# Performance work log

Hardware: AMD Instinct MI355X
Metric: run time of the kernel (lower is better)

## Reference

```python
import jax, jax.numpy as jnp
import numpy as np

B, C, T = 4, 512, 4096
N2 = 32          # d_state // 2 complex modes
H = 2048         # hidden_channels
EPS = 1e-5


def setup_inputs() -> dict:
    key = jax.random.key(0)
    ks = jax.random.split(key, 8)
    dt_min, dt_max = 1e-3, 1e-1
    log_dt = jax.random.uniform(ks[1], (C,)) * (np.log(dt_max) - np.log(dt_min)) + np.log(dt_min)
    return {
        "x": jax.random.normal(ks[0], (B, C, T), jnp.float32),
        # ChannelwiseLayerNorm affine params
        "gamma": jnp.ones((C,), jnp.float32),
        "beta": jnp.zeros((C,), jnp.float32),
        # S4D kernel params (standard S4D-Lin init)
        "log_dt": log_dt.astype(jnp.float32),
        "C_re": jax.random.normal(ks[2], (C, N2), jnp.float32),
        "C_im": jax.random.normal(ks[3], (C, N2), jnp.float32),
        "log_A_real": jnp.log(0.5 * jnp.ones((C, N2), jnp.float32)),
        "A_imag": jnp.tile(jnp.pi * jnp.arange(N2, dtype=jnp.float32), (C, 1)),
        "D": jax.random.normal(ks[4], (C,), jnp.float32),
        # S4D output linear (Conv1d k=1 -> 2C, then GLU over channels)
        "Wo": jax.random.normal(ks[5], (2 * C, C), jnp.float32) / np.sqrt(C),
        "bo": jnp.zeros((2 * C,), jnp.float32),
        # FC MLP: Linear(C->H), PReLU(H), Linear(H->C)
        "W1": jax.random.normal(ks[6], (H, C), jnp.float32) / np.sqrt(C),
        "b1": jnp.zeros((H,), jnp.float32),
        "prelu_a": 0.25 * jnp.ones((H,), jnp.float32),
        "W2": jax.random.normal(ks[7], (C, H), jnp.float32) / np.sqrt(H),
        "b2": jnp.zeros((C,), jnp.float32),
    }


def reference(x, gamma, beta, log_dt, C_re, C_im, log_A_real, A_imag, D,
              Wo, bo, W1, b1, prelu_a, W2, b2):
    # ---- ChannelwiseLayerNorm over the channel dim of [B, C, T] ----
    mean = jnp.mean(x, axis=1, keepdims=True)
    var = jnp.var(x, axis=1, keepdims=True)
    u = gamma[None, :, None] * (x - mean) * jax.lax.rsqrt(var + EPS) + beta[None, :, None]

    # ---- S4D: diagonal SSM kernel via Vandermonde, applied by FFT conv ----
    L = x.shape[-1]
    dt = jnp.exp(log_dt)[:, None]                       # [C, 1]
    A = -jnp.exp(log_A_real) + 1j * A_imag              # [C, N2] complex diag
    dtA = A * dt                                        # [C, N2]
    Cd = (C_re + 1j * C_im) * (jnp.exp(dtA) - 1.0) / A  # discretized C (ZOH)
    vand = jnp.exp(dtA[..., None] * jnp.arange(L, dtype=jnp.float32))  # [C, N2, L]
    K = 2.0 * jnp.einsum('hn,hnl->hl', Cd, vand).real   # [C, L]

    k_f = jnp.fft.rfft(K, n=2 * L)                      # [C, L+1]
    u_f = jnp.fft.rfft(u, n=2 * L)                      # [B, C, L+1]
    y = jnp.fft.irfft(u_f * k_f, n=2 * L)[..., :L]      # causal conv
    y = y + u * D[None, :, None]                        # skip connection
    y = jax.nn.gelu(y, approximate=False)
    # output linear (1x1 conv to 2C) + GLU over channel dim
    z = jnp.einsum('oc,bct->bot', Wo, y) + bo[None, :, None]
    y = z[:, :C] * jax.nn.sigmoid(z[:, C:])             # [B, C, T]

    # ---- FC MLP with PReLU (per hidden channel) ----
    y = y.transpose(0, 2, 1)                            # [B, T, C]
    h = y @ W1.T + b1                                   # [B, T, H]
    h = jnp.where(h >= 0, h, prelu_a * h)
    y = h @ W2.T + b2                                   # [B, T, C]

    return x + y.transpose(0, 2, 1)                     # residual, [B, C, T]
```

## Files before the change

### kernel.cpp

```cpp
#include <hip/hip_runtime.h>
#include <math.h>

#define BB 4
#define CC 512
#define TT 4096
#define NN2 32
#define HH 2048

typedef __bf16 bf8v __attribute__((ext_vector_type(8)));
typedef __bf16 bf4v __attribute__((ext_vector_type(4)));
typedef float  f4v  __attribute__((ext_vector_type(4)));
typedef unsigned short u16x8 __attribute__((ext_vector_type(8)));

__device__ __forceinline__ void gload16(const void* g, void* l){
  __builtin_amdgcn_global_load_lds(
      (const __attribute__((address_space(1))) unsigned int*)g,
      (__attribute__((address_space(3))) unsigned int*)l, 16, 0, 0);
}
__device__ __forceinline__ float fast_gelu(float v){
  float x2 = v*v;
  float x  = 0.7978845608f*v*fmaf(0.044715f, x2, 1.0f);
  float t  = __expf(2.0f*x);
  return v - v*__builtin_amdgcn_rcpf(1.0f + t);
}
__device__ __forceinline__ float fast_sigmoid(float g){
  return __builtin_amdgcn_rcpf(1.0f + __expf(-g));
}
__device__ __forceinline__ unsigned short bfbits(float v){
  __bf16 h = (__bf16)v;
  return __builtin_bit_cast(unsigned short, h);
}

__global__ __launch_bounds__(256) void ln_kernel(
    const float* __restrict__ x, const float* __restrict__ gamma,
    const float* __restrict__ beta, __bf16* __restrict__ u)
{
  int tile = blockIdx.x & 127;
  int b    = blockIdx.x >> 7;
  int tsl = threadIdx.x & 7;
  int cg  = threadIdx.x >> 3;
  const float4* xp = (const float4*)(x + (size_t)b*CC*TT + tile*32) + tsl;
  float4 cv[16];
  float4 s = {0,0,0,0}, s2 = {0,0,0,0};
  #pragma unroll
  for (int j = 0; j < 16; ++j){
    float4 v = xp[(size_t)(cg*16 + j)*(TT/4)];
    cv[j] = v;
    s.x += v.x; s.y += v.y; s.z += v.z; s.w += v.w;
    s2.x = fmaf(v.x,v.x,s2.x); s2.y = fmaf(v.y,v.y,s2.y);
    s2.z = fmaf(v.z,v.z,s2.z); s2.w = fmaf(v.w,v.w,s2.w);
  }
  __shared__ float4 ls[32][8], ls2[32][8], mean_s[8], inv_s[8];
  ls[cg][tsl] = s; ls2[cg][tsl] = s2;
  __syncthreads();
  if (threadIdx.x < 8){
    float4 ss = {0,0,0,0}, ss2 = {0,0,0,0};
    #pragma unroll
    for (int g2 = 0; g2 < 32; ++g2){
      float4 a = ls[g2][threadIdx.x], b2 = ls2[g2][threadIdx.x];
      ss.x+=a.x; ss.y+=a.y; ss.z+=a.z; ss.w+=a.w;
      ss2.x+=b2.x; ss2.y+=b2.y; ss2.z+=b2.z; ss2.w+=b2.w;
    }
    float4 mn, iv;
    mn.x = ss.x*(1.f/CC); mn.y = ss.y*(1.f/CC); mn.z = ss.z*(1.f/CC); mn.w = ss.w*(1.f/CC);
    iv.x = rsqrtf(ss2.x*(1.f/CC) - mn.x*mn.x + 1e-5f);
    iv.y = rsqrtf(ss2.y*(1.f/CC) - mn.y*mn.y + 1e-5f);
    iv.z = rsqrtf(ss2.z*(1.f/CC) - mn.z*mn.z + 1e-5f);
    iv.w = rsqrtf(ss2.w*(1.f/CC) - mn.w*mn.w + 1e-5f);
    mean_s[threadIdx.x] = mn; inv_s[threadIdx.x] = iv;
  }
  __syncthreads();
  float4 mn = mean_s[tsl], iv = inv_s[tsl];
  __bf16* up = u + (size_t)b*CC*TT + tile*32 + tsl*4;
  #pragma unroll
  for (int j = 0; j < 16; ++j){
    int c = cg*16 + j;
    float4 v = cv[j];
    float gi = gamma[c], be = beta[c];
    bf4v o;
    o[0] = (__bf16)fmaf(gi*iv.x, v.x - mn.x, be);
    o[1] = (__bf16)fmaf(gi*iv.y, v.y - mn.y, be);
    o[2] = (__bf16)fmaf(gi*iv.z, v.z - mn.z, be);
    o[3] = (__bf16)fmaf(gi*iv.w, v.w - mn.w, be);
    *(bf4v*)&up[(size_t)c*TT] = o;
  }
}

__global__ __launch_bounds__(256) void build_mats(
    const float* __restrict__ log_dt, const float* __restrict__ C_re,
    const float* __restrict__ C_im, const float* __restrict__ log_A_real,
    const float* __restrict__ A_imag, const float* __restrict__ Dp,
    __bf16* __restrict__ Tt, __bf16* __restrict__ V, __bf16* __restrict__ B2)
{
  __shared__ float cpart[4][64][33];
  __shared__ float kk[4][65];
  const int wv = threadIdx.x >> 6, lane = threadIdx.x & 63;
  const int c = blockIdx.x*4 + wv;
  const int m = lane & 31;
  float dt = expf(log_dt[c]);
  float Ar = -expf(log_A_real[c*NN2+m]);
  float Ai = A_imag[c*NN2+m];
  float er = expf(Ar*dt);
  float sw_, cw_; sincosf(Ai*dt, &sw_, &cw_);
  float wre = er*cw_, wim = er*sw_;
  float nr = wre-1.f, ni = wim;
  float inv = 1.f/(Ar*Ar + Ai*Ai);
  float qr = (nr*Ar + ni*Ai)*inv;
  float qi = (ni*Ar - nr*Ai)*inv;
  float Cr = C_re[c*NN2+m], Ci = C_im[c*NN2+m];
  float okr =  2.f*(Cr*qr - Ci*qi);
  float oki = -2.f*(Cr*qi + Ci*qr);
  __bf16* Ttc = Tt + (size_t)c*4096;
  __bf16* Vc  = V  + (size_t)c*4096;
  __bf16* B2c = B2 + (size_t)c*4096;
  if (lane < 32){
    float pre = 1.f, pim = 0.f;
    for (int l = 0; l <= 64; ++l){
      if (l <= 63){
        Vc[(2*m)*64   + (63-l)] = (__bf16)pre;
        Vc[(2*m+1)*64 + (63-l)] = (__bf16)pim;
      }
      float cR = fmaf(okr, pre,  oki*pim);
      float cQ = fmaf(oki, pre, -okr*pim);
      if (l <= 63) cpart[wv][l][m] = cR;
      if (l >= 1){
        B2c[(l-1)*64 + 2*m]   = (__bf16)cR;
        B2c[(l-1)*64 + 2*m+1] = (__bf16)cQ;
      }
      float npre = wre*pre - wim*pim;
      float npim = wre*pim + wim*pre;
      pre = npre; pim = npim;
    }
  }
  __syncthreads();
  float s = 0.f;
  #pragma unroll
  for (int mm = 0; mm < 32; ++mm) s += cpart[wv][lane][mm];
  if (lane == 0) s += Dp[c];
  kk[wv][lane] = s;
  __syncthreads();
  const int n = lane;
  #pragma unroll
  for (int kb = 0; kb < 8; ++kb){
    u16x8 v;
    #pragma unroll
    for (int e = 0; e < 8; ++e){
      int k = kb*8 + e;
      v[e] = bfbits((n >= k) ? kk[wv][n-k] : 0.f);
    }
    *(u16x8*)&Ttc[n*64 + kb*8] = v;
  }
}

__global__ __launch_bounds__(128) void s4dm_kernel(
    const __bf16* __restrict__ u, const float* __restrict__ log_dt,
    const float* __restrict__ log_A_real, const float* __restrict__ A_imag,
    const __bf16* __restrict__ Tt, const __bf16* __restrict__ V,
    const __bf16* __restrict__ B2, __bf16* __restrict__ gout)
{
  __shared__ __align__(16) float gbuf[2][64][66];
  __shared__ __align__(16) unsigned short s0buf[2][64][72];
  const int wv = threadIdx.x >> 6, l = threadIdx.x & 63;
  const int lr = l & 15, q = l >> 4;
  const int seq = blockIdx.x*2 + wv;
  const int c = seq & (CC-1);
  const __bf16* Up  = u  + (size_t)seq*TT;
  const __bf16* Ttc = Tt + (size_t)c*4096;
  const __bf16* Vc  = V  + (size_t)c*4096;
  const __bf16* B2c = B2 + (size_t)c*4096;

  f4v acc[4][4];
  #pragma unroll
  for (int a=0;a<4;++a)
    #pragma unroll
    for (int b=0;b<4;++b)
      #pragma unroll
      for (int r=0;r<4;++r) acc[a][b][r] = 0.f;

  #pragma unroll
  for (int kw = 0; kw < 2; ++kw){
    bf8v af[4], bv[4];
    #pragma unroll
    for (int mt=0;mt<4;++mt)
      af[mt] = *(const bf8v*)(Up + (mt*16+lr)*64 + kw*32 + q*8);
    #pragma unroll
    for (int nt=0;nt<4;++nt)
      bv[nt] = *(const bf8v*)(Vc + (nt*16+lr)*64 + kw*32 + q*8);
    #pragma unroll
    for (int mt=0;mt<4;++mt)
      #pragma unroll
      for (int nt=0;nt<4;++nt)
        acc[mt][nt] = __builtin_amdgcn_mfma_f32_16x16x32_bf16(af[mt], bv[nt], acc[mt][nt], 0,0,0);
  }
  #pragma unroll
  for (int mt=0;mt<4;++mt)
    #pragma unroll
    for (int nt=0;nt<4;++nt)
      #pragma unroll
      for (int r=0;r<4;++r)
        gbuf[wv][mt*16 + q*4 + r][nt*16 + lr] = acc[mt][nt][r];
  __syncthreads();

  if (l < 32){
    const int m = l;
    float dt = expf(log_dt[c]);
    float Ar = -expf(log_A_real[c*NN2+m]);
    float Ai = A_imag[c*NN2+m];
    float er = expf(Ar*dt);
    float sw_, cw_; sincosf(Ai*dt, &sw_, &cw_);
    float wr_ = er*cw_, wi_ = er*sw_;
    #pragma unroll
    for (int sq2=0;sq2<6;++sq2){
      float a=wr_, b=wi_;
      wr_ = a*a - b*b; wi_ = 2.f*a*b;
    }
    float S0r=0.f, S0i=0.f;
    for (int j=0;j<64;++j){
      float gr = gbuf[wv][j][2*m], gi = gbuf[wv][j][2*m+1];
      s0buf[wv][j][2*m]   = bfbits(S0r);
      s0buf[wv][j][2*m+1] = bfbits(S0i);
      float nRe = fmaf(wr_, S0r, fmaf(-wi_, S0i, gr));
      float nIm = fmaf(wr_, S0i, fmaf( wi_, S0r, gi));
      S0r = nRe; S0i = nIm;
    }
  }
  __syncthreads();

  #pragma unroll
  for (int a=0;a<4;++a)
    #pragma unroll
    for (int b=0;b<4;++b)
      #pragma unroll
      for (int r=0;r<4;++r) acc[a][b][r] = 0.f;
  #pragma unroll
  for (int kw = 0; kw < 2; ++kw){
    bf8v af[4], bv[4];
    #pragma unroll
    for (int mt=0;mt<4;++mt)
      af[mt] = *(const bf8v*)(Up + (mt*16+lr)*64 + kw*32 + q*8);
    #pragma unroll
    for (int nt=0;nt<4;++nt)
      bv[nt] = *(const bf8v*)(Ttc + (nt*16+lr)*64 + kw*32 + q*8);
    #pragma unroll
    for (int mt=0;mt<4;++mt)
      #pragma unroll
      for (int nt=0;nt<4;++nt)
        acc[mt][nt] = __builtin_amdgcn_mfma_f32_16x16x32_bf16(af[mt], bv[nt], acc[mt][nt], 0,0,0);
  }
  #pragma unroll
  for (int kw = 0; kw < 2; ++kw){
    bf8v af[4], bv[4];
    #pragma unroll
    for (int mt=0;mt<4;++mt)
      af[mt] = *(const bf8v*)&s0buf[wv][mt*16+lr][kw*32 + q*8];
    #pragma unroll
    for (int nt=0;nt<4;++nt)
      bv[nt] = *(const bf8v*)(B2c + (nt*16+lr)*64 + kw*32 + q*8);
    #pragma unroll
    for (int mt=0;mt<4;++mt)
      #pragma unroll
      for (int nt=0;nt<4;++nt)
        acc[mt][nt] = __builtin_amdgcn_mfma_f32_16x16x32_bf16(af[mt], bv[nt], acc[mt][nt], 0,0,0);
  }
  __syncthreads();

  unsigned short (*ybuf)[72] = (unsigned short(*)[72])&gbuf[wv][0][0];
  #pragma unroll
  for (int mt=0;mt<4;++mt)
    #pragma unroll
    for (int nt=0;nt<4;++nt)
      #pragma unroll
      for (int r=0;r<4;++r)
        ybuf[mt*16 + q*4 + r][nt*16 + lr] = bfbits(fast_gelu(acc[mt][nt][r]));
  __syncthreads();
  u16x8* dst = (u16x8*)(gout + (size_t)seq*TT);
  for (int i = l; i < 512; i += 64){
    int row = i >> 3, cq = i & 7;
    dst[i] = *(const u16x8*)&ybuf[row][cq*8];
  }
}

__global__ __launch_bounds__(256) void tr_kernel(const __bf16* __restrict__ gin,
                                                 __bf16* __restrict__ gout)
{
  __shared__ __align__(16) unsigned short ts[64][72];
  int bt = blockIdx.x;
  int bc = blockIdx.y;
  int b  = blockIdx.z;
  int tid = threadIdx.x;
  const __bf16* gp = gin + ((size_t)b*CC + bc*64)*TT + (size_t)bt*64;
  for (int i = tid; i < 512; i += 256){
    int c = i >> 3, tq = i & 7;
    u16x8 v = *(const u16x8*)(gp + (size_t)c*TT + tq*8);
    #pragma unroll
    for (int s = 0; s < 8; ++s) ts[tq*8+s][c] = v[s];
  }
  __syncthreads();
  __bf16* op = gout + ((size_t)b*TT + bt*64)*CC + bc*64;
  for (int i = tid; i < 512; i += 256){
    int t = i >> 3, cq = i & 7;
    u16x8 v = *(const u16x8*)&ts[t][cq*8];
    *(u16x8*)(op + (size_t)t*CC + cq*8) = v;
  }
}

__global__ __launch_bounds__(256) void cvt_kernel(const float4* __restrict__ in,
                                                  bf4v* __restrict__ out, int n4)
{
  int i = blockIdx.x*256 + threadIdx.x;
  if (i < n4){
    float4 v = in[i];
    bf4v o; o[0]=(__bf16)v.x; o[1]=(__bf16)v.y; o[2]=(__bf16)v.z; o[3]=(__bf16)v.w;
    out[i] = o;
  }
}

template<int MODE>
__global__ __launch_bounds__(256) void mm_kernel(
    const __bf16* __restrict__ Aw, const __bf16* __restrict__ Bt,
    const float* __restrict__ bias, const float* __restrict__ aux,
    void* __restrict__ outp)
{
  constexpr int K  = (MODE==2) ? 2048 : 512;
  constexpr int NT = K/64;
  constexpr int LOGGM = (MODE==1) ? 4 : 2;
  constexpr int GM = 1 << LOGGM;

  __shared__ __align__(16) __bf16 As[128*64];
  __shared__ __align__(16) __bf16 Bs[128*64];
  __shared__ __align__(16) __bf16 As2[(MODE==0)?128*64:8];

  const int bid = blockIdx.x;
  const int X = bid & 7, L = bid >> 3;
  const int m0 = (L & (GM-1)) * 128;
  const int n0 = (X*16 + (L >> LOGGM)) * 128;

  const int tid = threadIdx.x;
  const int l = tid & 63;
  const int lr = l & 15, kh = l >> 4;
  const int w = tid >> 6;
  const int wr = w >> 1, wc = w & 1;
  const int swk = lr & 7;

  f4v acc[4][4];
  f4v acc2[(MODE==0)?4:1][(MODE==0)?4:1];
  #pragma unroll
  for (int a=0;a<4;++a)
    #pragma unroll
    for (int b=0;b<4;++b)
      #pragma unroll
      for (int r=0;r<4;++r) acc[a][b][r] = 0.f;
  if constexpr (MODE==0){
    #pragma unroll
    for (int a=0;a<4;++a)
      #pragma unroll
      for (int b=0;b<4;++b)
        #pragma unroll
        for (int r=0;r<4;++r) acc2[a][b][r] = 0.f;
  }

  const char* pA  = (const char*)Aw;
  const char* pA2 = (const char*)(Aw + (size_t)CC*K);
  const char* pB  = (const char*)Bt;

  int offA[4], offB[4];
  #pragma unroll
  for (int i = 0; i < 4; ++i){
    int cch = i*256 + tid;
    int row = cch >> 3;
    int pos = cch & 7;
    int qq  = pos ^ (row & 7);
    offA[i] = ((m0 + row)*K + qq*8)*2;
    offB[i] = ((n0 + row)*K + qq*8)*2;
  }

  #pragma unroll 1
  for (int kt = 0; kt < NT; ++kt){
    #pragma unroll
    for (int i = 0; i < 4; ++i){
      int cch = i*256 + tid;
      gload16(pA + (size_t)offA[i] + kt*128, (char*)As + cch*16);
      gload16(pB + (size_t)offB[i] + kt*128, (char*)Bs + cch*16);
      if constexpr (MODE==0)
        gload16(pA2 + (size_t)offA[i] + kt*128, (char*)As2 + cch*16);
    }
    __syncthreads();

    #pragma unroll
    for (int kk2 = 0; kk2 < 2; ++kk2){
      const int coff = ((kk2*4 + kh) ^ swk) * 16;
      bf8v af[4], bv4[4];
      #pragma unroll
      for (int mi=0;mi<4;++mi){
        int row = wr*64 + mi*16 + lr;
        af[mi] = *(const bf8v*)((const char*)As + row*128 + coff);
      }
      #pragma unroll
      for (int ni=0;ni<4;++ni){
        int row = wc*64 + ni*16 + lr;
        bv4[ni] = *(const bf8v*)((const char*)Bs + row*128 + coff);
      }
      if constexpr (MODE==0){
        bf8v af2[4];
        #pragma unroll
        for (int mi=0;mi<4;++mi){
          int row = wr*64 + mi*16 + lr;
          af2[mi] = *(const bf8v*)((const char*)As2 + row*128 + coff);
        }
        #pragma unroll
        for (int mi=0;mi<4;++mi)
          #pragma unroll
          for (int ni=0;ni<4;++ni){
            acc [mi][ni] = __builtin_amdgcn_mfma_f32_16x16x32_bf16(af [mi], bv4[ni], acc [mi][ni], 0,0,0);
            acc2[mi][ni] = __builtin_amdgcn_mfma_f32_16x16x32_bf16(af2[mi], bv4[ni], acc2[mi][ni], 0,0,0);
          }
      } else {
        #pragma unroll
        for (int mi=0;mi<4;++mi)
          #pragma unroll
          for (int ni=0;ni<4;++ni)
            acc[mi][ni] = __builtin_amdgcn_mfma_f32_16x16x32_bf16(af[mi], bv4[ni], acc[mi][ni], 0,0,0);
      }
    }
    __syncthreads();
  }

  if constexpr (MODE==0 || MODE==1){
    const int COUT = (MODE==0) ? CC : HH;
    __bf16* O = (__bf16*)outp;
    #pragma unroll
    for (int mi=0;mi<4;++mi){
      int m = m0 + wr*64 + mi*16 + kh*4;
      float4 bi = *(const float4*)&bias[m];
      float bia[4] = {bi.x, bi.y, bi.z, bi.w};
      float gta[4], paa[4];
      if constexpr (MODE==0){
        float4 bg = *(const float4*)&bias[CC + m];
        gta[0]=bg.x; gta[1]=bg.y; gta[2]=bg.z; gta[3]=bg.w;
      } else {
        float4 pa = *(const float4*)&aux[m];
        paa[0]=pa.x; paa[1]=pa.y; paa[2]=pa.z; paa[3]=pa.w;
      }
      #pragma unroll
      for (int ni=0;ni<4;++ni){
        int tok = n0 + wc*64 + ni*16 + lr;
        bf4v o;
        #pragma unroll
        for (int r=0;r<4;++r){
          float v = acc[mi][ni][r] + bia[r];
          if constexpr (MODE==0){
            float gate = acc2[mi][ni][r] + gta[r];
            v = v * fast_sigmoid(gate);
          } else {
            v = (v >= 0.f) ? v : paa[r]*v;
          }
          o[r] = (__bf16)v;
        }
        *(bf4v*)&O[(size_t)tok*COUT + m] = o;
      }
    }
  } else {
    float* O = (float*)outp;
    #pragma unroll
    for (int mi=0;mi<4;++mi){
      int chb = m0 + wr*64 + mi*16 + kh*4;
      float4 bi = *(const float4*)&bias[chb];
      float bia[4] = {bi.x, bi.y, bi.z, bi.w};
      #pragma unroll
      for (int ni=0;ni<4;++ni){
        int tok = n0 + wc*64 + ni*16 + lr;
        int b = tok >> 12, t = tok & 4095;
        size_t rb = ((size_t)(b*CC + chb))*TT + t;
        #pragma unroll
        for (int r=0;r<4;++r)
          O[rb + (size_t)r*TT] = acc[mi][ni][r] + bia[r] + aux[rb + (size_t)r*TT];
      }
    }
  }
}

extern "C" void kernel_launch(void* const* d_in, const int* in_sizes, int n_in,
                              void* d_out, int out_size, void* d_ws, size_t ws_size,
                              hipStream_t stream)
{
  const float* x          = (const float*)d_in[0];
  const float* gamma      = (const float*)d_in[1];
  const float* beta       = (const float*)d_in[2];
  const float* log_dt     = (const float*)d_in[3];
  const float* C_re       = (const float*)d_in[4];
  const float* C_im       = (const float*)d_in[5];
  const float* log_A_real = (const float*)d_in[6];
  const float* A_imag     = (const float*)d_in[7];
  const float* Dp         = (const float*)d_in[8];
  const float* Wo         = (const float*)d_in[9];
  const float* bo         = (const float*)d_in[10];
  const float* W1         = (const float*)d_in[11];
  const float* b1         = (const float*)d_in[12];
  const float* prelu_a    = (const float*)d_in[13];
  const float* W2         = (const float*)d_in[14];
  const float* b2         = (const float*)d_in[15];
  float* out = (float*)d_out;

  char* base = (char*)d_ws;
  const size_t SEGB = (size_t)BB*CC*TT*2;
  __bf16* u_bf  = (__bf16*)(base);
  __bf16* glu   = (__bf16*)(base);
  __bf16* g_cm  = (__bf16*)(base + SEGB);
  __bf16* g_tm  = (__bf16*)(base + 2*SEGB);
  __bf16* h     = (__bf16*)(base + SEGB);
  __bf16* Tt_all = (__bf16*)(base + 2*SEGB);
  __bf16* V_all  = Tt_all + (size_t)CC*4096;
  __bf16* B2_all = V_all  + (size_t)CC*4096;
  __bf16* Wo_bf = (__bf16*)(base + 5*SEGB);
  __bf16* W1_bf = Wo_bf + (size_t)2*CC*CC;
  __bf16* W2_bf = W1_bf + (size_t)HH*CC;

  cvt_kernel<<<dim3((2*CC*CC/4 + 255)/256), 256, 0, stream>>>((const float4*)Wo, (bf4v*)Wo_bf, 2*CC*CC/4);
  cvt_kernel<<<dim3((HH*CC/4 + 255)/256), 256, 0, stream>>>((const float4*)W1, (bf4v*)W1_bf, HH*CC/4);
  cvt_kernel<<<dim3((CC*HH/4 + 255)/256), 256, 0, stream>>>((const float4*)W2, (bf4v*)W2_bf, CC*HH/4);

  build_mats<<<dim3(CC/4), 256, 0, stream>>>(log_dt, C_re, C_im, log_A_real,
                                             A_imag, Dp, Tt_all, V_all, B2_all);
  ln_kernel<<<dim3(BB*(TT/32)), 256, 0, stream>>>(x, gamma, beta, u_bf);
  s4dm_kernel<<<dim3((BB*CC)/2), 128, 0, stream>>>(u_bf, log_dt, log_A_real, A_imag,
                                                   Tt_all, V_all, B2_all, g_cm);
  tr_kernel<<<dim3(TT/64, CC/64, BB), 256, 0, stream>>>(g_cm, g_tm);

  mm_kernel<0><<<dim3(4*128),  256, 0, stream>>>(Wo_bf, g_tm, bo, nullptr, (void*)glu);
  mm_kernel<1><<<dim3(16*128), 256, 0, stream>>>(W1_bf, glu, b1, prelu_a, (void*)h);
  mm_kernel<2><<<dim3(4*128),  256, 0, stream>>>(W2_bf, h, b2, x, (void*)out);
}
```

Baseline: 207.7 us.

## Add double-buffered 8-wave 256-row GEMM kernel for MLP layers

Splits the gated Wo GEMM into its own kernel and adds a new 512-thread GEMM kernel for the two MLP layers. It uses 256-row tiles, double-buffered LDS, and loads for later k-tiles issued between MFMA phases, with explicit vmcnt waits and raised wave priority. For the second MLP GEMM the operands are swapped so tokens run along M, which lets the residual add use float4 reads and writes. The goal is to hide global-load latency and raise MFMA utilisation. The cost is a larger LDS footprint, higher register pressure and hand-written synchronisation that is fragile.

After: 221.0 us. 1.06x slower.

```diff
diff --git a/kernel.cpp b/kernel.cpp
--- a/kernel.cpp
+++ b/kernel.cpp
@@ -315,25 +315,20 @@
   }
 }
 
-template<int MODE>
-__global__ __launch_bounds__(256) void mm_kernel(
+__global__ __launch_bounds__(256) void mm0_kernel(
     const __bf16* __restrict__ Aw, const __bf16* __restrict__ Bt,
-    const float* __restrict__ bias, const float* __restrict__ aux,
-    void* __restrict__ outp)
-{
-  constexpr int K  = (MODE==2) ? 2048 : 512;
+    const float* __restrict__ bias, void* __restrict__ outp)
+{
+  constexpr int K  = 512;
   constexpr int NT = K/64;
-  constexpr int LOGGM = (MODE==1) ? 4 : 2;
-  constexpr int GM = 1 << LOGGM;
-
   __shared__ __align__(16) __bf16 As[128*64];
   __shared__ __align__(16) __bf16 Bs[128*64];
-  __shared__ __align__(16) __bf16 As2[(MODE==0)?128*64:8];
+  __shared__ __align__(16) __bf16 As2[128*64];
 
   const int bid = blockIdx.x;
   const int X = bid & 7, L = bid >> 3;
-  const int m0 = (L & (GM-1)) * 128;
-  const int n0 = (X*16 + (L >> LOGGM)) * 128;
+  const int m0 = (L & 3) * 128;
+  const int n0 = (X*16 + (L >> 2)) * 128;
 
   const int tid = threadIdx.x;
   const int l = tid & 63;
@@ -342,22 +337,13 @@
   const int wr = w >> 1, wc = w & 1;
   const int swk = lr & 7;
 
-  f4v acc[4][4];
-  f4v acc2[(MODE==0)?4:1][(MODE==0)?4:1];
+  f4v acc[4][4], acc2[4][4];
   #pragma unroll
   for (int a=0;a<4;++a)
     #pragma unroll
     for (int b=0;b<4;++b)
       #pragma unroll
-      for (int r=0;r<4;++r) acc[a][b][r] = 0.f;
-  if constexpr (MODE==0){
-    #pragma unroll
-    for (int a=0;a<4;++a)
-      #pragma unroll
-      for (int b=0;b<4;++b)
-        #pragma unroll
-        for (int r=0;r<4;++r) acc2[a][b][r] = 0.f;
-  }
+      for (int r=0;r<4;++r){ acc[a][b][r] = 0.f; acc2[a][b][r] = 0.f; }
 
   const char* pA  = (const char*)Aw;
   const char* pA2 = (const char*)(Aw + (size_t)CC*K);
@@ -381,99 +367,224 @@
       int cch = i*256 + tid;
       gload16(pA + (size_t)offA[i] + kt*128, (char*)As + cch*16);
       gload16(pB + (size_t)offB[i] + kt*128, (char*)Bs + cch*16);
-      if constexpr (MODE==0)
-        gload16(pA2 + (size_t)offA[i] + kt*128, (char*)As2 + cch*16);
+      gload16(pA2 + (size_t)offA[i] + kt*128, (char*)As2 + cch*16);
     }
     __syncthreads();
-
     #pragma unroll
     for (int kk2 = 0; kk2 < 2; ++kk2){
       const int coff = ((kk2*4 + kh) ^ swk) * 16;
-      bf8v af[4], bv4[4];
+      bf8v af[4], bv4[4], af2[4];
       #pragma unroll
       for (int mi=0;mi<4;++mi){
         int row = wr*64 + mi*16 + lr;
-        af[mi] = *(const bf8v*)((const char*)As + row*128 + coff);
+        af[mi]  = *(const bf8v*)((const char*)As  + row*128 + coff);
+        af2[mi] = *(const bf8v*)((const char*)As2 + row*128 + coff);
       }
       #pragma unroll
       for (int ni=0;ni<4;++ni){
         int row = wc*64 + ni*16 + lr;
         bv4[ni] = *(const bf8v*)((const char*)Bs + row*128 + coff);
       }
-      if constexpr (MODE==0){
-        bf8v af2[4];
+      #pragma unroll
+      for (int mi=0;mi<4;++mi)
         #pragma unroll
-        for (int mi=0;mi<4;++mi){
-          int row = wr*64 + mi*16 + lr;
-          af2[mi] = *(const bf8v*)((const char*)As2 + row*128 + coff);
+        for (int ni=0;ni<4;++ni){
+          acc [mi][ni] = __builtin_amdgcn_mfma_f32_16x16x32_bf16(af [mi], bv4[ni], acc [mi][ni], 0,0,0);
+          acc2[mi][ni] = __builtin_amdgcn_mfma_f32_16x16x32_bf16(af2[mi], bv4[ni], acc2[mi][ni], 0,0,0);
         }
+    }
+    __syncthreads();
+  }
+
+  __bf16* O = (__bf16*)outp;
+  #pragma unroll
+  for (int mi=0;mi<4;++mi){
+    int m = m0 + wr*64 + mi*16 + kh*4;
+    float4 bi = *(const float4*)&bias[m];
+    float bia[4] = {bi.x, bi.y, bi.z, bi.w};
+    float4 bg = *(const float4*)&bias[CC + m];
+    float gta[4] = {bg.x, bg.y, bg.z, bg.w};
+    #pragma unroll
+    for (int ni=0;ni<4;++ni){
+      int tok = n0 + wc*64 + ni*16 + lr;
+      bf4v o;
+      #pragma unroll
+      for (int r=0;r<4;++r){
+        float v = acc[mi][ni][r] + bia[r];
+        float gate = acc2[mi][ni][r] + gta[r];
+        o[r] = (__bf16)(v * fast_sigmoid(gate));
+      }
+      *(bf4v*)&O[(size_t)tok*CC + m] = o;
+    }
+  }
+}
+
+template<int MODE>
+__global__ __launch_bounds__(512, 2) void mm8_kernel(
+    const __bf16* __restrict__ Aw, const __bf16* __restrict__ Bt,
+    const float* __restrict__ bias, const float* __restrict__ aux,
+    void* __restrict__ outp)
+{
+  constexpr int K   = (MODE==2) ? 2048 : 512;
+  constexpr int NT  = K/64;
+  constexpr int BN  = (MODE==1) ? 256 : 128;
+  constexpr int BNH = BN/2;
+  constexpr int FN  = BN/64;
+  constexpr int FN2 = FN/2;
+  constexpr int LB  = BNH/64;
+  constexpr int CNT = 2 + LB;
+
+  __shared__ __align__(16) __bf16 As[2*2*128*64];
+  __shared__ __align__(16) __bf16 Bs[2*2*BNH*64];
+
+  const int bid = blockIdx.x;
+  const int X = bid & 7, L = bid >> 3;
+  int mt, nt;
+  if constexpr (MODE==1){ mt = L & 7;       nt = X*8 + (L >> 3); }
+  else                  { nt = L & 3;       mt = X*8 + (L >> 2); }
+  const int m0 = mt*256, n0 = nt*BN;
+
+  const int tid = threadIdx.x;
+  const int l = tid & 63;
+  const int lr = l & 15, kh = l >> 4;
+  const int w = tid >> 6;
+  const int wm = w & 1, wn = w >> 1;
+  const int swk = lr & 7;
+
+  f4v acc[8][FN];
+  #pragma unroll
+  for (int f=0; f<8; ++f)
+    #pragma unroll
+    for (int g=0; g<FN; ++g)
+      #pragma unroll
+      for (int r=0; r<4; ++r) acc[f][g][r] = 0.f;
+
+  const char* pA = (const char*)Aw;
+  const char* pB = (const char*)Bt;
+
+  auto stageA = [&](int slot, int hA, int t){
+    #pragma unroll
+    for (int j=0; j<2; ++j){
+      int cch = j*512 + tid;
+      int rl = cch >> 3, pos = cch & 7;
+      int qq = pos ^ (rl & 7);
+      gload16(pA + ((size_t)(m0 + hA*128 + rl)*K + t*64 + qq*8)*2,
+              (char*)As + ((slot*2 + hA)*(128*64) + cch*8)*2);
+    }
+  };
+  auto stageB = [&](int slot, int hB, int t){
+    #pragma unroll
+    for (int j=0; j<LB; ++j){
+      int cch = j*512 + tid;
+      int rl = cch >> 3, pos = cch & 7;
+      int qq = pos ^ (rl & 7);
+      gload16(pB + ((size_t)(n0 + hB*BNH + rl)*K + t*64 + qq*8)*2,
+              (char*)Bs + ((slot*2 + hB)*(BNH*64) + cch*8)*2);
+    }
+  };
+
+  stageA(0,0,0); stageB(0,0,0); stageA(0,1,0); stageB(0,1,0);
+  stageA(1,0,1); stageB(1,0,1);
+  asm volatile("s_waitcnt vmcnt(%0)" :: "n"(CNT) : "memory");
+  __builtin_amdgcn_s_barrier();
+
+  #pragma unroll 1
+  for (int i = 0; i < NT/2; ++i){
+    const int T0 = 2*i;
+    #pragma unroll
+    for (int p = 0; p < 8; ++p){
+      const int hA = (p>>1)&1, hB = p&1;
+      const int slot = (T0 + (p>>2)) & 1;
+      const char* Ab = (const char*)As + (size_t)(slot*2 + hA)*(128*64*2);
+      const char* Bb = (const char*)Bs + (size_t)(slot*2 + hB)*(BNH*64*2);
+      bf8v a[4][2], b[FN2][2];
+      #pragma unroll
+      for (int fi=0; fi<4; ++fi){
+        const int rl = fi*32 + wm*16 + lr;
         #pragma unroll
-        for (int mi=0;mi<4;++mi)
+        for (int kk=0; kk<2; ++kk)
+          a[fi][kk] = *(const bf8v*)(Ab + rl*128 + (((kk*4+kh)^swk)*16));
+      }
+      #pragma unroll
+      for (int gi=0; gi<FN2; ++gi){
+        const int cl = gi*64 + wn*16 + lr;
+        #pragma unroll
+        for (int kk=0; kk<2; ++kk)
+          b[gi][kk] = *(const bf8v*)(Bb + cl*128 + (((kk*4+kh)^swk)*16));
+      }
+      if      (p==0)  stageA((T0+1)&1, 1, T0+1);
+      else if (p==1)  stageB((T0+1)&1, 1, T0+1);
+      else if (p==2){ if (T0+2 < NT) stageA((T0+2)&1, 0, T0+2); }
+      else if (p==3){ if (T0+2 < NT) stageB((T0+2)&1, 0, T0+2); }
+      else if (p==4){ if (T0+2 < NT) stageA((T0+2)&1, 1, T0+2); }
+      else if (p==5){ if (T0+2 < NT) stageB((T0+2)&1, 1, T0+2); }
+      else if (p==6){ if (T0+3 < NT) stageA((T0+3)&1, 0, T0+3); }
+      else          { if (T0+3 < NT) stageB((T0+3)&1, 0, T0+3); }
+      __builtin_amdgcn_s_barrier();
+      asm volatile("s_waitcnt lgkmcnt(0)" ::: "memory");
+      __builtin_amdgcn_sched_barrier(0);
+      __builtin_amdgcn_s_setprio(1);
+      #pragma unroll
+      for (int fi=0; fi<4; ++fi)
+        #pragma unroll
+        for (int gi=0; gi<FN2; ++gi)
           #pragma unroll
-          for (int ni=0;ni<4;++ni){
-            acc [mi][ni] = __builtin_amdgcn_mfma_f32_16x16x32_bf16(af [mi], bv4[ni], acc [mi][ni], 0,0,0);
-            acc2[mi][ni] = __builtin_amdgcn_mfma_f32_16x16x32_bf16(af2[mi], bv4[ni], acc2[mi][ni], 0,0,0);
-          }
-      } else {
-        #pragma unroll
-        for (int mi=0;mi<4;++mi)
-          #pragma unroll
-          for (int ni=0;ni<4;++ni)
-            acc[mi][ni] = __builtin_amdgcn_mfma_f32_16x16x32_bf16(af[mi], bv4[ni], acc[mi][ni], 0,0,0);
-      }
-    }
-    __syncthreads();
-  }
-
-  if constexpr (MODE==0 || MODE==1){
-    const int COUT = (MODE==0) ? CC : HH;
+          for (int kk=0; kk<2; ++kk)
+            acc[hA*4+fi][hB*FN2+gi] =
+              __builtin_amdgcn_mfma_f32_16x16x32_bf16(a[fi][kk], b[gi][kk],
+                                                      acc[hA*4+fi][hB*FN2+gi], 0,0,0);
+      __builtin_amdgcn_s_setprio(0);
+      if (p==3){
+        if (T0+2 < NT) asm volatile("s_waitcnt vmcnt(%0)" :: "n"(CNT) : "memory");
+        else           asm volatile("s_waitcnt vmcnt(0)" ::: "memory");
+      }
+      if (p==7){
+        if (T0+3 < NT) asm volatile("s_waitcnt vmcnt(%0)" :: "n"(CNT) : "memory");
+        else           asm volatile("s_waitcnt vmcnt(0)" ::: "memory");
+      }
+      __builtin_amdgcn_s_barrier();
+    }
+  }
+
+  if constexpr (MODE==1){
     __bf16* O = (__bf16*)outp;
     #pragma unroll
-    for (int mi=0;mi<4;++mi){
-      int m = m0 + wr*64 + mi*16 + kh*4;
+    for (int f=0; f<8; ++f){
+      int m = m0 + f*32 + wm*16 + kh*4;
       float4 bi = *(const float4*)&bias[m];
       float bia[4] = {bi.x, bi.y, bi.z, bi.w};
-      float gta[4], paa[4];
-      if constexpr (MODE==0){
-        float4 bg = *(const float4*)&bias[CC + m];
-        gta[0]=bg.x; gta[1]=bg.y; gta[2]=bg.z; gta[3]=bg.w;
-      } else {
-        float4 pa = *(const float4*)&aux[m];
-        paa[0]=pa.x; paa[1]=pa.y; paa[2]=pa.z; paa[3]=pa.w;
-      }
-      #pragma unroll
-      for (int ni=0;ni<4;++ni){
-        int tok = n0 + wc*64 + ni*16 + lr;
+      float4 pa = *(const float4*)&aux[m];
+      float paa[4] = {pa.x, pa.y, pa.z, pa.w};
+      #pragma unroll
+      for (int g=0; g<FN; ++g){
+        int tok = n0 + g*64 + wn*16 + lr;
         bf4v o;
         #pragma unroll
-        for (int r=0;r<4;++r){
-          float v = acc[mi][ni][r] + bia[r];
-          if constexpr (MODE==0){
-            float gate = acc2[mi][ni][r] + gta[r];
-            v = v * fast_sigmoid(gate);
-          } else {
-            v = (v >= 0.f) ? v : paa[r]*v;
-          }
-          o[r] = (__bf16)v;
+        for (int r=0; r<4; ++r){
+          float v = acc[f][g][r] + bia[r];
+          o[r] = (__bf16)((v >= 0.f) ? v : paa[r]*v);
         }
-        *(bf4v*)&O[(size_t)tok*COUT + m] = o;
+        *(bf4v*)&O[(size_t)tok*HH + m] = o;
       }
     }
   } else {
     float* O = (float*)outp;
     #pragma unroll
-    for (int mi=0;mi<4;++mi){
-      int chb = m0 + wr*64 + mi*16 + kh*4;
-      float4 bi = *(const float4*)&bias[chb];
-      float bia[4] = {bi.x, bi.y, bi.z, bi.w};
-      #pragma unroll
-      for (int ni=0;ni<4;++ni){
-        int tok = n0 + wc*64 + ni*16 + lr;
-        int b = tok >> 12, t = tok & 4095;
-        size_t rb = ((size_t)(b*CC + chb))*TT + t;
-        #pragma unroll
-        for (int r=0;r<4;++r)
-          O[rb + (size_t)r*TT] = acc[mi][ni][r] + bia[r] + aux[rb + (size_t)r*TT];
+    for (int f=0; f<8; ++f){
+      int tok = m0 + f*32 + wm*16 + kh*4;
+      int bq = tok >> 12, t = tok & 4095;
+      #pragma unroll
+      for (int g=0; g<FN; ++g){
+        int ch = n0 + g*64 + wn*16 + lr;
+        float bb = bias[ch];
+        size_t rb = ((size_t)(bq*CC + ch))*TT + t;
+        float4 xr = *(const float4*)&aux[rb];
+        float4 o;
+        o.x = acc[f][g][0] + bb + xr.x;
+        o.y = acc[f][g][1] + bb + xr.y;
+        o.z = acc[f][g][2] + bb + xr.z;
+        o.w = acc[f][g][3] + bb + xr.w;
+        *(float4*)&O[rb] = o;
       }
     }
   }
@@ -526,7 +637,7 @@
                                                    Tt_all, V_all, B2_all, g_cm);
   tr_kernel<<<dim3(TT/64, CC/64, BB), 256, 0, stream>>>(g_cm, g_tm);
 
-  mm_kernel<0><<<dim3(4*128),  256, 0, stream>>>(Wo_bf, g_tm, bo, nullptr, (void*)glu);
-  mm_kernel<1><<<dim3(16*128), 256, 0, stream>>>(W1_bf, glu, b1, prelu_a, (void*)h);
-  mm_kernel<2><<<dim3(4*128),  256, 0, stream>>>(W2_bf, h, b2, x, (void*)out);
-}
+  mm0_kernel<<<dim3(4*128), 256, 0, stream>>>(Wo_bf, g_tm, bo, (void*)glu);
+  mm8_kernel<1><<<dim3(512), 512, 0, stream>>>(W1_bf, glu, b1, prelu_a, (void*)h);
+  mm8_kernel<2><<<dim3(256), 512, 0, stream>>>(h, W2_bf, b2, x, (void*)out);
+}
```
